# Optimization experiments

Hardware: AMD Instinct MI355X
Metric: run time of the kernel (lower is better)

## Reference

```python
import jax, jax.numpy as jnp
import numpy as np
import math

EMB, SEQ, OUT, FF, B = 1024, 1024, 2, 1024, 32
EPS = 1e-5


def _build_pe(seq_len, emb_dim):
    # Faithful to the buggy torch loop: for even i, pe[pos,i] is first set to sin
    # then immediately overwritten by cos(pos / 10000**(2*(i+1)/emb_dim));
    # odd indices are never written (stay 0).
    pos = np.arange(seq_len, dtype=np.float64)[:, None]
    i = np.arange(0, emb_dim, 2, dtype=np.float64)[None, :]
    pe = np.zeros((seq_len, emb_dim), dtype=np.float32)
    pe[:, ::2] = np.cos(pos / 10000.0 ** (2.0 * (i + 1.0) / emb_dim)).astype(np.float32)
    return jnp.asarray(pe)[None]  # [1, S, D]


def setup_inputs() -> dict:
    key = jax.random.key(0)
    ks = jax.random.split(key, 24)
    std = 0.02
    W = lambda k, o, i: jax.random.normal(k, (o, i), jnp.float32) * std
    b = lambda k, o: jax.random.normal(k, (o,), jnp.float32) * std
    return {
        "x": jax.random.normal(ks[0], (B, SEQ, EMB), jnp.float32),
        "pe": _build_pe(SEQ, EMB),
        "ln1_g": jnp.ones((EMB,), jnp.float32), "ln1_b": jnp.zeros((EMB,), jnp.float32),
        "Wq": W(ks[1], EMB, EMB), "bq": b(ks[2], EMB),
        "Wk": W(ks[3], EMB, EMB), "bk": b(ks[4], EMB),
        "Wv": W(ks[5], EMB, EMB), "bv": b(ks[6], EMB),
        "Wo": W(ks[7], EMB, EMB), "bo": b(ks[8], EMB),
        "ln2_g": jnp.ones((EMB,), jnp.float32), "ln2_b": jnp.zeros((EMB,), jnp.float32),
        "W1": W(ks[9], FF, EMB), "b1": b(ks[10], FF),
        "W2": W(ks[11], EMB, FF), "b2": b(ks[12], EMB),
        "Wc": W(ks[13], OUT, EMB), "bc": b(ks[14], OUT),
    }


def _ln(x, g, bias):
    mu = jnp.mean(x, axis=-1, keepdims=True)
    var = jnp.mean(jnp.square(x - mu), axis=-1, keepdims=True)
    return (x - mu) * jax.lax.rsqrt(var + EPS) * g + bias


def _block(x, ln1_g, ln1_b, Wq, bq, Wk, bk, Wv, bv, Wo, bo, ln2_g, ln2_b, W1, b1, W2, b2):
    h = _ln(x, ln1_g, ln1_b)
    q = h @ Wq.T + bq
    k = h @ Wk.T + bk
    v = h @ Wv.T + bv
    scores = jnp.einsum('bqd,bkd->bqk', q, k) / math.sqrt(EMB)
    w = jax.nn.softmax(scores, axis=-1)  # [B,S,S]
    attn = jnp.einsum('bqk,bkd->bqd', w, v) @ Wo.T + bo
    x2 = x + attn  # dropout is identity in eval
    h2 = _ln(x2, ln2_g, ln2_b)
    ff = jax.nn.relu(h2 @ W1.T + b1) @ W2.T + b2
    return x2 + ff, w


def reference(x, pe, ln1_g, ln1_b, Wq, bq, Wk, bk, Wv, bv, Wo, bo, ln2_g, ln2_b, W1, b1, W2, b2, Wc, bc):
    x1 = math.sqrt(EMB) * x + pe
    # Original forward applies block net2_1 twice (net2_2 is unused) -> reuse params.
    p = (ln1_g, ln1_b, Wq, bq, Wk, bk, Wv, bv, Wo, bo, ln2_g, ln2_b, W1, b1, W2, b2)
    x2_1, w1 = _block(x1, *p)
    x2_2, w2 = _block(x2_1, *p)
    logits = x2_2[:, 0, :] @ Wc.T + bc
    return logits, w1, w2
```

## Files before the change

kernel.cpp:

```cpp
#include <hip/hip_runtime.h>
#include <cstdint>


#define AS1 __attribute__((address_space(1)))
#define AS3 __attribute__((address_space(3)))

typedef __attribute__((ext_vector_type(8))) short bf16x8;
typedef __attribute__((ext_vector_type(4))) float f32x4;
typedef __attribute__((ext_vector_type(4))) unsigned short us4;

__device__ __forceinline__ unsigned short f2bf(float f) {
  unsigned int u = __builtin_bit_cast(unsigned int, f);
  u += 0x7fffu + ((u >> 16) & 1u);
  return (unsigned short)(u >> 16);
}
__device__ __forceinline__ float bf2f(unsigned short h) {
  return __builtin_bit_cast(float, (unsigned int)h << 16);
}

__device__ __forceinline__ void gload_lds16(const void* g, void* l) {
  auto gp = reinterpret_cast<AS1 unsigned int*>(reinterpret_cast<uintptr_t>(g));
  auto lp = reinterpret_cast<AS3 unsigned int*>(reinterpret_cast<uintptr_t>(l));
  __builtin_amdgcn_global_load_lds(gp, lp, 16, 0, 0);
}

enum { M_BF16 = 0, M_RELU = 1, M_QKV = 2, M_SCBF = 3, M_RESID = 4 };


#define MFMA_QUAD(qi, qj)                                                          \
  do {                                                                             \
    _Pragma("unroll") for (int i2 = 0; i2 < 4; ++i2) {                             \
      _Pragma("unroll") for (int j2 = 0; j2 < 2; ++j2) {                           \
        f32x4& c = acc[(qi) * 4 + i2][(qj) * 2 + j2];                              \
        c = __builtin_amdgcn_mfma_f32_16x16x32_bf16(aF[(qi) * 4 + i2][0],          \
                                                    bF[(qj) * 2 + j2][0], c, 0, 0, 0); \
        c = __builtin_amdgcn_mfma_f32_16x16x32_bf16(aF[(qi) * 4 + i2][1],          \
                                                    bF[(qj) * 2 + j2][1], c, 0, 0, 0); \
      }                                                                            \
    }                                                                              \
  } while (0)

template<int MODE>
__global__ __launch_bounds__(512, 2) void gemm_bt(
    const unsigned short* __restrict__ A, long long sAb,
    const unsigned short* __restrict__ B, long long sBb,
    const float* __restrict__ bias,
    const float* __restrict__ resid,
    float* __restrict__ outF,
    unsigned short* __restrict__ outBF,
    long long sOb, int N, int K, float scale)
{
  __shared__ __align__(16) unsigned short lds[65536];
  const int t    = threadIdx.x;
  const int w    = t >> 6;
  const int lane = t & 63;
  const int quad = lane >> 4;
  const int l16  = lane & 15;
  const int l7   = l16 & 7;
  const int wm   = w >> 2;
  const int wn   = w & 3;
  const int bz   = blockIdx.z;
  const unsigned short* Ab = A + (long long)bz * sAb;
  const unsigned short* Bb = B + (long long)bz * sBb;
  const int m0 = blockIdx.y * 256;
  const int n0 = blockIdx.x * 256;

  const int sr8  = lane >> 3;
  const int gseg = ((lane & 7) ^ sr8) << 3;
  const unsigned short* aSrc = Ab + (long long)(m0 + w * 8 + sr8) * K + gseg;
  const unsigned short* bSrc = Bb + (long long)(n0 + w * 8 + sr8) * K + gseg;
  const int ldsW = w << 9;

  const int aOff = (wm * 128 + l16) * 64;
  const int bOff = 16384 + (wn * 64 + l16) * 64;
  const int seg0 = (quad ^ l7) << 3;
  const int seg1 = ((quad + 4) ^ l7) << 3;

  const int NG = K >> 6;

  const f32x4 zero = {0.f, 0.f, 0.f, 0.f};
  f32x4 acc[8][4];
#pragma unroll
  for (int i = 0; i < 8; ++i)
#pragma unroll
    for (int j = 0; j < 4; ++j) acc[i][j] = zero;

  bf16x8 aF[8][2];
  bf16x8 bF[4][2];

#define STAGE_A(kt, h) do {                                                        \
    const unsigned short* _s = aSrc + (long long)(h) * 128 * K + (kt) * 64;        \
    unsigned short* _d = &lds[(((kt) & 1) << 15) + ((h) << 13) + ldsW];            \
    gload_lds16(_s, _d);                                                           \
    gload_lds16(_s + 64 * (long long)K, _d + 4096);                                \
  } while (0)
#define STAGE_B(kt, h) do {                                                        \
    const unsigned short* _s = bSrc + (long long)(h) * 128 * K + (kt) * 64;        \
    unsigned short* _d = &lds[(((kt) & 1) << 15) + 16384 + ((h) << 13) + ldsW];    \
    gload_lds16(_s, _d);                                                           \
    gload_lds16(_s + 64 * (long long)K, _d + 4096);                                \
  } while (0)

  STAGE_A(0, 0); STAGE_A(0, 1); STAGE_B(0, 0); STAGE_B(0, 1);
  STAGE_A(1, 0); STAGE_A(1, 1);
  asm volatile("s_waitcnt vmcnt(4)" ::: "memory");
  __builtin_amdgcn_s_barrier();
  asm volatile("" ::: "memory");

#pragma unroll 1
  for (int g = 0; g < NG; ++g) {
    const unsigned short* As = &lds[(g & 1) << 15];

#pragma unroll
    for (int i2 = 0; i2 < 4; ++i2) {
      aF[i2][0] = *(const bf16x8*)&As[aOff + i2 * 1024 + seg0];
      aF[i2][1] = *(const bf16x8*)&As[aOff + i2 * 1024 + seg1];
    }
#pragma unroll
    for (int j2 = 0; j2 < 2; ++j2) {
      bF[j2][0] = *(const bf16x8*)&As[bOff + j2 * 1024 + seg0];
      bF[j2][1] = *(const bf16x8*)&As[bOff + j2 * 1024 + seg1];
    }
    if (g + 1 < NG) STAGE_B(g + 1, 0);
    __builtin_amdgcn_s_barrier();
    asm volatile("s_waitcnt lgkmcnt(0)" ::: "memory");
    __builtin_amdgcn_s_setprio(1);
    MFMA_QUAD(0, 0);
    __builtin_amdgcn_s_setprio(0);
    __builtin_amdgcn_s_barrier();
    asm volatile("" ::: "memory");

#pragma unroll
    for (int i2 = 0; i2 < 4; ++i2) {
      aF[4 + i2][0] = *(const bf16x8*)&As[aOff + (4 + i2) * 1024 + seg0];
      aF[4 + i2][1] = *(const bf16x8*)&As[aOff + (4 + i2) * 1024 + seg1];
    }
    if (g + 1 < NG) STAGE_B(g + 1, 1);
    __builtin_amdgcn_s_barrier();
    asm volatile("s_waitcnt lgkmcnt(0)" ::: "memory");
    __builtin_amdgcn_s_setprio(1);
    MFMA_QUAD(1, 0);
    __builtin_amdgcn_s_setprio(0);
    __builtin_amdgcn_s_barrier();
    asm volatile("" ::: "memory");

#pragma unroll
    for (int j2 = 0; j2 < 2; ++j2) {
      bF[2 + j2][0] = *(const bf16x8*)&As[bOff + (2 + j2) * 1024 + seg0];
      bF[2 + j2][1] = *(const bf16x8*)&As[bOff + (2 + j2) * 1024 + seg1];
    }
    if (g + 2 < NG) STAGE_A(g + 2, 0);
    __builtin_amdgcn_s_barrier();
    asm volatile("s_waitcnt lgkmcnt(0)" ::: "memory");
    __builtin_amdgcn_s_setprio(1);
    MFMA_QUAD(1, 1);
    __builtin_amdgcn_s_setprio(0);
    __builtin_amdgcn_s_barrier();
    asm volatile("" ::: "memory");

    if (g + 2 < NG) STAGE_A(g + 2, 1);
    if (g >= NG - 2) {
      asm volatile("s_waitcnt vmcnt(0)" ::: "memory");
    } else {
      asm volatile("s_waitcnt vmcnt(4)" ::: "memory");
    }
    __builtin_amdgcn_s_barrier();
    __builtin_amdgcn_s_setprio(1);
    MFMA_QUAD(0, 1);
    __builtin_amdgcn_s_setprio(0);
    __builtin_amdgcn_s_barrier();
    asm volatile("" ::: "memory");
  }

#undef STAGE_A
#undef STAGE_B

#pragma unroll
  for (int i = 0; i < 8; ++i) {
    const int mt = m0 + wm * 128 + i * 16 + quad * 4;
#pragma unroll
    for (int j = 0; j < 4; ++j) {
      const int nt = n0 + wn * 64 + j * 16 + l16;
      f32x4 d = acc[i][j];
      if (MODE == M_BF16 || MODE == M_RELU) {
        const float bv = bias ? bias[nt] : 0.0f;
#pragma unroll
        for (int r = 0; r < 4; ++r) {
          float v = d[r] + bv;
          if (MODE == M_RELU) v = fmaxf(v, 0.0f);
          outBF[(long long)bz * sOb + (long long)(mt + r) * N + nt] = f2bf(v);
        }
      } else if (MODE == M_SCBF) {
#pragma unroll
        for (int r = 0; r < 4; ++r)
          outBF[(long long)bz * sOb + (long long)(mt + r) * N + nt] = f2bf(d[r] * scale);
      } else if (MODE == M_RESID) {
        const float bv = bias[nt];
#pragma unroll
        for (int r = 0; r < 4; ++r) {
          const long long idx = (long long)(mt + r) * N + nt;
          outF[idx] = resid[idx] + d[r] + bv;
        }
      } else if (MODE == M_QKV) {
        const int seg = n0 >> 10;
        const int ntl = nt - (seg << 10);
        const float bv = bias[nt];
        if (seg < 2) {
          unsigned short* dst = outBF + (long long)seg * 33554432LL;
#pragma unroll
          for (int r = 0; r < 4; ++r)
            dst[(long long)(mt + r) * 1024 + ntl] = f2bf(d[r] + bv);
        } else {
          unsigned short* dst = outBF + 2LL * 33554432LL;
          us4 pk;
#pragma unroll
          for (int r = 0; r < 4; ++r) pk[r] = f2bf(d[r] + bv);
          const int b = mt >> 10;
          const int s = mt & 1023;
          *(us4*)&dst[(long long)b * 1048576 + (long long)ntl * 1024 + s] = pk;
        }
      }
    }
  }
}

template<int EMBED>
__global__ __launch_bounds__(256) void ln_kernel(
    const float* __restrict__ xin, const float* __restrict__ pe,
    float* __restrict__ x1out,
    const float* __restrict__ g, const float* __restrict__ bb,
    unsigned short* __restrict__ hout)
{
  __shared__ float red[8];
  const long long row = blockIdx.x;
  const int t = threadIdx.x, lane = t & 63, w = t >> 6;
  float4 v = *(const float4*)(xin + row * 1024 + t * 4);
  if (EMBED) {
    const int s = (int)(row & 1023);
    float4 p = *(const float4*)(pe + (long long)s * 1024 + t * 4);
    v.x = 32.0f * v.x + p.x;
    v.y = 32.0f * v.y + p.y;
    v.z = 32.0f * v.z + p.z;
    v.w = 32.0f * v.w + p.w;
    *(float4*)(x1out + row * 1024 + t * 4) = v;
  }
  float sum = v.x + v.y + v.z + v.w;
  float sq  = v.x * v.x + v.y * v.y + v.z * v.z + v.w * v.w;
#pragma unroll
  for (int off = 32; off > 0; off >>= 1) {
    sum += __shfl_down(sum, off, 64);
    sq  += __shfl_down(sq,  off, 64);
  }
  if (lane == 0) { red[w] = sum; red[4 + w] = sq; }
  __syncthreads();
  sum = red[0] + red[1] + red[2] + red[3];
  sq  = red[4] + red[5] + red[6] + red[7];
  const float mu  = sum * (1.0f / 1024.0f);
  const float var = sq * (1.0f / 1024.0f) - mu * mu;
  const float rs  = rsqrtf(var + 1e-5f);
  float4 gg = *(const float4*)(g + t * 4);
  float4 bv = *(const float4*)(bb + t * 4);
  us4 h;
  h[0] = f2bf((v.x - mu) * rs * gg.x + bv.x);
  h[1] = f2bf((v.y - mu) * rs * gg.y + bv.y);
  h[2] = f2bf((v.z - mu) * rs * gg.z + bv.z);
  h[3] = f2bf((v.w - mu) * rs * gg.w + bv.w);
  *(us4*)(hout + row * 1024 + t * 4) = h;
}

__global__ __launch_bounds__(256) void softmax_kernel(
    const unsigned short* __restrict__ sbf,
    float* __restrict__ wout, unsigned short* __restrict__ wbf)
{
  __shared__ float red[8];
  const long long row = blockIdx.x;
  const int t = threadIdx.x, lane = t & 63, w = t >> 6;
  us4 sv = *(const us4*)(sbf + row * 1024 + t * 4);
  float4 v;
  v.x = bf2f(sv[0]); v.y = bf2f(sv[1]); v.z = bf2f(sv[2]); v.w = bf2f(sv[3]);
  float mx = fmaxf(fmaxf(v.x, v.y), fmaxf(v.z, v.w));
#pragma unroll
  for (int off = 32; off > 0; off >>= 1) mx = fmaxf(mx, __shfl_down(mx, off, 64));
  if (lane == 0) red[w] = mx;
  __syncthreads();
  mx = fmaxf(fmaxf(red[0], red[1]), fmaxf(red[2], red[3]));
  __syncthreads();
  const float e0 = __expf(v.x - mx), e1 = __expf(v.y - mx);
  const float e2 = __expf(v.z - mx), e3 = __expf(v.w - mx);
  float s = e0 + e1 + e2 + e3;
#pragma unroll
  for (int off = 32; off > 0; off >>= 1) s += __shfl_down(s, off, 64);
  if (lane == 0) red[w] = s;
  __syncthreads();
  s = red[0] + red[1] + red[2] + red[3];
  const float inv = 1.0f / s;
  float4 o; o.x = e0 * inv; o.y = e1 * inv; o.z = e2 * inv; o.w = e3 * inv;
  *(float4*)(wout + row * 1024 + t * 4) = o;
  us4 ob;
  ob[0] = f2bf(o.x); ob[1] = f2bf(o.y); ob[2] = f2bf(o.z); ob[3] = f2bf(o.w);
  *(us4*)(wbf + row * 1024 + t * 4) = ob;
}

__global__ __launch_bounds__(256) void prep_kernel(
    const float* __restrict__ Wq, const float* __restrict__ Wk, const float* __restrict__ Wv,
    const float* __restrict__ Wo, const float* __restrict__ W1, const float* __restrict__ W2,
    const float* __restrict__ bq, const float* __restrict__ bk, const float* __restrict__ bv,
    unsigned short* __restrict__ qkvw, unsigned short* __restrict__ Wo_bf,
    unsigned short* __restrict__ W1_bf, unsigned short* __restrict__ W2_bf,
    float* __restrict__ qkvb)
{
  const int y = blockIdx.y;
  const long long i = blockIdx.x * 256 + threadIdx.x;
  if (y == 6) {
    if (i < 768) {
      const float* src = (i < 256) ? bq : (i < 512) ? bk : bv;
      float4 v = *(const float4*)(src + (i & 255) * 4);
      *(float4*)(qkvb + i * 4) = v;
    }
    return;
  }
  const float* src;
  unsigned short* dst;
  switch (y) {
    case 0: src = Wq; dst = qkvw;            break;
    case 1: src = Wk; dst = qkvw + 1048576;  break;
    case 2: src = Wv; dst = qkvw + 2097152;  break;
    case 3: src = Wo; dst = Wo_bf;           break;
    case 4: src = W1; dst = W1_bf;           break;
    default: src = W2; dst = W2_bf;          break;
  }
  float4 v = *(const float4*)(src + i * 4);
  us4 o;
  o[0] = f2bf(v.x); o[1] = f2bf(v.y); o[2] = f2bf(v.z); o[3] = f2bf(v.w);
  *(us4*)(dst + i * 4) = o;
}

__global__ __launch_bounds__(256) void logits_kernel(
    const float* __restrict__ x, const float* __restrict__ Wc,
    const float* __restrict__ bc, float* __restrict__ out)
{
  __shared__ float red[4];
  const int blk = blockIdx.x;
  const int b = blk >> 1, o = blk & 1;
  const int t = threadIdx.x, lane = t & 63, w = t >> 6;
  const float* xr = x + (long long)b * 1048576;
  const float* wr = Wc + o * 1024;
  float4 xv = *(const float4*)(xr + t * 4);
  float4 wv = *(const float4*)(wr + t * 4);
  float s = xv.x * wv.x + xv.y * wv.y + xv.z * wv.z + xv.w * wv.w;
#pragma unroll
  for (int off = 32; off > 0; off >>= 1) s += __shfl_down(s, off, 64);
  if (lane == 0) red[w] = s;
  __syncthreads();
  if (t == 0) out[blk] = red[0] + red[1] + red[2] + red[3] + bc[o];
}

extern "C" void kernel_launch(void* const* d_in, const int* in_sizes, int n_in,
                              void* d_out, int out_size, void* d_ws, size_t ws_size,
                              hipStream_t stream)
{
  const float* x    = (const float*)d_in[0];
  const float* pe   = (const float*)d_in[1];
  const float* ln1g = (const float*)d_in[2];
  const float* ln1b = (const float*)d_in[3];
  const float* Wq   = (const float*)d_in[4];
  const float* bq   = (const float*)d_in[5];
  const float* Wk   = (const float*)d_in[6];
  const float* bk   = (const float*)d_in[7];
  const float* Wv   = (const float*)d_in[8];
  const float* bv   = (const float*)d_in[9];
  const float* Wo   = (const float*)d_in[10];
  const float* bo   = (const float*)d_in[11];
  const float* ln2g = (const float*)d_in[12];
  const float* ln2b = (const float*)d_in[13];
  const float* W1   = (const float*)d_in[14];
  const float* b1   = (const float*)d_in[15];
  const float* W2   = (const float*)d_in[16];
  const float* b2   = (const float*)d_in[17];
  const float* Wc   = (const float*)d_in[18];
  const float* bc   = (const float*)d_in[19];
  float* out = (float*)d_out;

  char* ws = (char*)d_ws;
  float*          xbuf  = (float*)ws;
  unsigned short* h_bf  = (unsigned short*)(ws + 134217728LL);
  unsigned short* q_bf  = (unsigned short*)(ws + 134217728LL + 1 * 67108864LL);
  unsigned short* k_bf  = (unsigned short*)(ws + 134217728LL + 2 * 67108864LL);
  unsigned short* vT_bf = (unsigned short*)(ws + 134217728LL + 3 * 67108864LL);
  unsigned short* wts   = (unsigned short*)(ws + 134217728LL + 4 * 67108864LL);
  unsigned short* QKV_bf = wts;
  unsigned short* Wo_bf  = wts + 3LL * 1048576;
  unsigned short* W1_bf  = wts + 4LL * 1048576;
  unsigned short* W2_bf  = wts + 5LL * 1048576;
  float*          qkvb   = (float*)(wts + 6LL * 1048576);
  unsigned short* sc_bf   = h_bf;
  unsigned short* w_bf    = k_bf;
  unsigned short* attn_bf = q_bf;
  unsigned short* ff1_bf  = vT_bf;

  const dim3 blk(256);
  const dim3 blkG(512);
  prep_kernel<<<dim3(1024, 7), blk, 0, stream>>>(Wq, Wk, Wv, Wo, W1, W2, bq, bk, bv,
                                                 QKV_bf, Wo_bf, W1_bf, W2_bf, qkvb);

  const dim3 gQKV(12, 128, 1);
  const dim3 gProj(4, 128, 1);
  const dim3 gAttn(4, 4, 32);

  for (int blkI = 0; blkI < 2; ++blkI) {
    float* wslot = out + 64 + (long long)blkI * 33554432LL;

    if (blkI == 0)
      ln_kernel<1><<<32768, blk, 0, stream>>>(x, pe, xbuf, ln1g, ln1b, h_bf);
    else
      ln_kernel<0><<<32768, blk, 0, stream>>>(xbuf, nullptr, nullptr, ln1g, ln1b, h_bf);

    gemm_bt<M_QKV><<<gQKV, blkG, 0, stream>>>(h_bf, 0, QKV_bf, 0, qkvb, nullptr,
                                              nullptr, q_bf, 0, 3072, 1024, 1.0f);

    gemm_bt<M_SCBF><<<gAttn, blkG, 0, stream>>>(q_bf, 1048576, k_bf, 1048576, nullptr,
                                                nullptr, nullptr, sc_bf, 1048576,
                                                1024, 1024, 0.03125f);
    softmax_kernel<<<32768, blk, 0, stream>>>(sc_bf, wslot, w_bf);

    gemm_bt<M_BF16><<<gAttn, blkG, 0, stream>>>(w_bf, 1048576, vT_bf, 1048576, nullptr,
                                                nullptr, nullptr, attn_bf, 1048576,
                                                1024, 1024, 1.0f);
    gemm_bt<M_RESID><<<gProj, blkG, 0, stream>>>(attn_bf, 0, Wo_bf, 0, bo, xbuf,
                                                 xbuf, nullptr, 0, 1024, 1024, 1.0f);

    ln_kernel<0><<<32768, blk, 0, stream>>>(xbuf, nullptr, nullptr, ln2g, ln2b, h_bf);
    gemm_bt<M_RELU><<<gProj, blkG, 0, stream>>>(h_bf, 0, W1_bf, 0, b1, nullptr,
                                                nullptr, ff1_bf, 0, 1024, 1024, 1.0f);
    gemm_bt<M_RESID><<<gProj, blkG, 0, stream>>>(ff1_bf, 0, W2_bf, 0, b2, xbuf,
                                                 xbuf, nullptr, 0, 1024, 1024, 1.0f);
  }

  logits_kernel<<<64, blk, 0, stream>>>(xbuf, Wc, bc, out);
  (void)in_sizes; (void)n_in; (void)out_size; (void)ws_size;
}
```

Before: 1.936 ms.

## Software-pipeline LDS fragment reads across MFMA quads and stage bf16 epilogue through LDS

Restructures the GEMM main loop so LDS fragment reads for the next quad, and for the next k-tile, are issued before the current MFMA quad runs. This halves the barriers per quad and unrolls the loop by two with explicit buffer offsets. The bf16 output epilogue now writes the tile into swizzled LDS and then emits 16-byte coalesced global stores instead of scattered 2-byte stores. The risks are LDS hazards from reusing the operand buffer for the epilogue and tighter vmcnt accounting, and the two-way unroll assumes an even NG.

New measurement: 3.079 ms. 1.59x slower.

```diff
diff --git a/kernel.cpp b/kernel.cpp
--- a/kernel.cpp
+++ b/kernel.cpp
@@ -8,6 +8,7 @@
 typedef __attribute__((ext_vector_type(8))) short bf16x8;
 typedef __attribute__((ext_vector_type(4))) float f32x4;
 typedef __attribute__((ext_vector_type(4))) unsigned short us4;
+typedef __attribute__((ext_vector_type(8))) unsigned short us8;
 
 __device__ __forceinline__ unsigned short f2bf(float f) {
   unsigned int u = __builtin_bit_cast(unsigned int, f);
@@ -25,7 +26,6 @@
 }
 
 enum { M_BF16 = 0, M_RELU = 1, M_QKV = 2, M_SCBF = 3, M_RESID = 4 };
-
 
 #define MFMA_QUAD(qi, qj)                                                          \
   do {                                                                             \
@@ -88,137 +88,172 @@
   bf16x8 aF[8][2];
   bf16x8 bF[4][2];
 
-#define STAGE_A(kt, h) do {                                                        \
+#define STAGE_A(kt, h, SL) do {                                                    \
     const unsigned short* _s = aSrc + (long long)(h) * 128 * K + (kt) * 64;        \
-    unsigned short* _d = &lds[(((kt) & 1) << 15) + ((h) << 13) + ldsW];            \
+    unsigned short* _d = &lds[(SL) + ((h) << 13) + ldsW];                          \
     gload_lds16(_s, _d);                                                           \
     gload_lds16(_s + 64 * (long long)K, _d + 4096);                                \
   } while (0)
-#define STAGE_B(kt, h) do {                                                        \
+#define STAGE_B(kt, h, SL) do {                                                    \
     const unsigned short* _s = bSrc + (long long)(h) * 128 * K + (kt) * 64;        \
-    unsigned short* _d = &lds[(((kt) & 1) << 15) + 16384 + ((h) << 13) + ldsW];    \
+    unsigned short* _d = &lds[(SL) + 16384 + ((h) << 13) + ldsW];                  \
     gload_lds16(_s, _d);                                                           \
     gload_lds16(_s + 64 * (long long)K, _d + 4096);                                \
   } while (0)
 
-  STAGE_A(0, 0); STAGE_A(0, 1); STAGE_B(0, 0); STAGE_B(0, 1);
-  STAGE_A(1, 0); STAGE_A(1, 1);
+#define READ_A03(SL)                                                               \
+    _Pragma("unroll") for (int i2 = 0; i2 < 4; ++i2) {                             \
+      aF[i2][0] = *(const bf16x8*)&lds[(SL) + aOff + i2 * 1024 + seg0];            \
+      aF[i2][1] = *(const bf16x8*)&lds[(SL) + aOff + i2 * 1024 + seg1];            \
+    }
+#define READ_A47(SL)                                                               \
+    _Pragma("unroll") for (int i2 = 0; i2 < 4; ++i2) {                             \
+      aF[4 + i2][0] = *(const bf16x8*)&lds[(SL) + aOff + (4 + i2) * 1024 + seg0];  \
+      aF[4 + i2][1] = *(const bf16x8*)&lds[(SL) + aOff + (4 + i2) * 1024 + seg1];  \
+    }
+#define READ_B01(SL)                                                               \
+    _Pragma("unroll") for (int j2 = 0; j2 < 2; ++j2) {                             \
+      bF[j2][0] = *(const bf16x8*)&lds[(SL) + bOff + j2 * 1024 + seg0];            \
+      bF[j2][1] = *(const bf16x8*)&lds[(SL) + bOff + j2 * 1024 + seg1];            \
+    }
+#define READ_B23(SL)                                                               \
+    _Pragma("unroll") for (int j2 = 0; j2 < 2; ++j2) {                             \
+      bF[2 + j2][0] = *(const bf16x8*)&lds[(SL) + bOff + (2 + j2) * 1024 + seg0];  \
+      bF[2 + j2][1] = *(const bf16x8*)&lds[(SL) + bOff + (2 + j2) * 1024 + seg1];  \
+    }
+
+#define KTILE(g, CUR, OTH)                                                         \
+  {                            \
+    __builtin_amdgcn_s_barrier();                                                  \
+    if ((g) + 1 < NG) STAGE_B((g) + 1, 0, OTH);                                    \
+    READ_B23(CUR)                                                                  \
+    __builtin_amdgcn_s_setprio(1);                                                 \
+    MFMA_QUAD(0, 0);                                                               \
+    __builtin_amdgcn_s_setprio(0);                                                 \
+    asm volatile("s_waitcnt lgkmcnt(0)" ::: "memory");                             \
+  }                                                                                \
+  {                                              \
+    __builtin_amdgcn_s_barrier();                                                  \
+    if ((g) + 1 < NG) STAGE_B((g) + 1, 1, OTH);                                    \
+    READ_A47(CUR)                                                                  \
+    __builtin_amdgcn_s_setprio(1);                                                 \
+    MFMA_QUAD(0, 1);                                                               \
+    __builtin_amdgcn_s_setprio(0);                                                 \
+    asm volatile("s_waitcnt lgkmcnt(0)" ::: "memory");                             \
+  }                                                                                \
+  {                                              \
+    __builtin_amdgcn_s_barrier();                                                  \
+    if ((g) + 2 < NG) STAGE_A((g) + 2, 0, CUR);                                    \
+    __builtin_amdgcn_s_setprio(1);                                                 \
+    MFMA_QUAD(1, 0);                                                               \
+    __builtin_amdgcn_s_setprio(0);                                                 \
+    if ((g) + 2 < NG) {                                                            \
+      asm volatile("s_waitcnt vmcnt(2) lgkmcnt(0)" ::: "memory");                  \
+    } else {                                                                       \
+      asm volatile("s_waitcnt vmcnt(0) lgkmcnt(0)" ::: "memory");                  \
+    }                                                                              \
+  }                                                                                \
+  {     \
+    __builtin_amdgcn_s_barrier();                                                  \
+    if ((g) + 2 < NG) STAGE_A((g) + 2, 1, CUR);                                    \
+    if ((g) + 1 < NG) {                                                            \
+      READ_A03(OTH)                                                                \
+      READ_B01(OTH)                                                                \
+    }                                                                              \
+    __builtin_amdgcn_s_setprio(1);                                                 \
+    MFMA_QUAD(1, 1);                                                               \
+    __builtin_amdgcn_s_setprio(0);                                                 \
+    asm volatile("s_waitcnt lgkmcnt(0)" ::: "memory");                             \
+  }
+
+  STAGE_A(0, 0, 0); STAGE_A(0, 1, 0); STAGE_B(0, 0, 0); STAGE_B(0, 1, 0);
+  STAGE_A(1, 0, 32768); STAGE_A(1, 1, 32768);
   asm volatile("s_waitcnt vmcnt(4)" ::: "memory");
   __builtin_amdgcn_s_barrier();
-  asm volatile("" ::: "memory");
+  READ_A03(0)
+  READ_B01(0)
+  asm volatile("s_waitcnt lgkmcnt(0)" ::: "memory");
 
 #pragma unroll 1
-  for (int g = 0; g < NG; ++g) {
-    const unsigned short* As = &lds[(g & 1) << 15];
-
-#pragma unroll
-    for (int i2 = 0; i2 < 4; ++i2) {
-      aF[i2][0] = *(const bf16x8*)&As[aOff + i2 * 1024 + seg0];
-      aF[i2][1] = *(const bf16x8*)&As[aOff + i2 * 1024 + seg1];
-    }
-#pragma unroll
-    for (int j2 = 0; j2 < 2; ++j2) {
-      bF[j2][0] = *(const bf16x8*)&As[bOff + j2 * 1024 + seg0];
-      bF[j2][1] = *(const bf16x8*)&As[bOff + j2 * 1024 + seg1];
-    }
-    if (g + 1 < NG) STAGE_B(g + 1, 0);
-    __builtin_amdgcn_s_barrier();
-    asm volatile("s_waitcnt lgkmcnt(0)" ::: "memory");
-    __builtin_amdgcn_s_setprio(1);
-    MFMA_QUAD(0, 0);
-    __builtin_amdgcn_s_setprio(0);
-    __builtin_amdgcn_s_barrier();
-    asm volatile("" ::: "memory");
-
-#pragma unroll
-    for (int i2 = 0; i2 < 4; ++i2) {
-      aF[4 + i2][0] = *(const bf16x8*)&As[aOff + (4 + i2) * 1024 + seg0];
-      aF[4 + i2][1] = *(const bf16x8*)&As[aOff + (4 + i2) * 1024 + seg1];
-    }
-    if (g + 1 < NG) STAGE_B(g + 1, 1);
-    __builtin_amdgcn_s_barrier();
-    asm volatile("s_waitcnt lgkmcnt(0)" ::: "memory");
-    __builtin_amdgcn_s_setprio(1);
-    MFMA_QUAD(1, 0);
-    __builtin_amdgcn_s_setprio(0);
-    __builtin_amdgcn_s_barrier();
-    asm volatile("" ::: "memory");
-
-#pragma unroll
-    for (int j2 = 0; j2 < 2; ++j2) {
-      bF[2 + j2][0] = *(const bf16x8*)&As[bOff + (2 + j2) * 1024 + seg0];
-      bF[2 + j2][1] = *(const bf16x8*)&As[bOff + (2 + j2) * 1024 + seg1];
-    }
-    if (g + 2 < NG) STAGE_A(g + 2, 0);
-    __builtin_amdgcn_s_barrier();
-    asm volatile("s_waitcnt lgkmcnt(0)" ::: "memory");
-    __builtin_amdgcn_s_setprio(1);
-    MFMA_QUAD(1, 1);
-    __builtin_amdgcn_s_setprio(0);
-    __builtin_amdgcn_s_barrier();
-    asm volatile("" ::: "memory");
-
-    if (g + 2 < NG) STAGE_A(g + 2, 1);
-    if (g >= NG - 2) {
-      asm volatile("s_waitcnt vmcnt(0)" ::: "memory");
-    } else {
-      asm volatile("s_waitcnt vmcnt(4)" ::: "memory");
-    }
-    __builtin_amdgcn_s_barrier();
-    __builtin_amdgcn_s_setprio(1);
-    MFMA_QUAD(0, 1);
-    __builtin_amdgcn_s_setprio(0);
-    __builtin_amdgcn_s_barrier();
-    asm volatile("" ::: "memory");
-  }
-
+  for (int g = 0; g < NG; g += 2) {
+    KTILE(g, 0, 32768)
+    KTILE(g + 1, 32768, 0)
+  }
+
+#undef KTILE
 #undef STAGE_A
 #undef STAGE_B
 
-#pragma unroll
-  for (int i = 0; i < 8; ++i) {
-    const int mt = m0 + wm * 128 + i * 16 + quad * 4;
-#pragma unroll
-    for (int j = 0; j < 4; ++j) {
-      const int nt = n0 + wn * 64 + j * 16 + l16;
-      f32x4 d = acc[i][j];
-      if (MODE == M_BF16 || MODE == M_RELU) {
-        const float bv = bias ? bias[nt] : 0.0f;
-#pragma unroll
-        for (int r = 0; r < 4; ++r) {
-          float v = d[r] + bv;
-          if (MODE == M_RELU) v = fmaxf(v, 0.0f);
-          outBF[(long long)bz * sOb + (long long)(mt + r) * N + nt] = f2bf(v);
-        }
-      } else if (MODE == M_SCBF) {
-#pragma unroll
-        for (int r = 0; r < 4; ++r)
-          outBF[(long long)bz * sOb + (long long)(mt + r) * N + nt] = f2bf(d[r] * scale);
-      } else if (MODE == M_RESID) {
+  const int segq = (MODE == M_QKV) ? (n0 >> 10) : 0;
+  if (MODE == M_QKV && segq == 2) {
+#pragma unroll
+    for (int i = 0; i < 8; ++i) {
+      const int mt = m0 + wm * 128 + i * 16 + quad * 4;
+#pragma unroll
+      for (int j = 0; j < 4; ++j) {
+        const int nt = n0 + wn * 64 + j * 16 + l16;
+        const int ntl = nt - 2048;
         const float bv = bias[nt];
+        f32x4 d = acc[i][j];
+        unsigned short* dst = outBF + 2LL * 33554432LL;
+        us4 pk;
+#pragma unroll
+        for (int r = 0; r < 4; ++r) pk[r] = f2bf(d[r] + bv);
+        const int b = mt >> 10;
+        const int s = mt & 1023;
+        *(us4*)&dst[(long long)b * 1048576 + (long long)ntl * 1024 + s] = pk;
+      }
+    }
+  } else if (MODE == M_RESID) {
+#pragma unroll
+    for (int i = 0; i < 8; ++i) {
+      const int mt = m0 + wm * 128 + i * 16 + quad * 4;
+#pragma unroll
+      for (int j = 0; j < 4; ++j) {
+        const int nt = n0 + wn * 64 + j * 16 + l16;
+        const float bv = bias[nt];
+        f32x4 d = acc[i][j];
 #pragma unroll
         for (int r = 0; r < 4; ++r) {
           const long long idx = (long long)(mt + r) * N + nt;
           outF[idx] = resid[idx] + d[r] + bv;
         }
-      } else if (MODE == M_QKV) {
-        const int seg = n0 >> 10;
-        const int ntl = nt - (seg << 10);
-        const float bv = bias[nt];
-        if (seg < 2) {
-          unsigned short* dst = outBF + (long long)seg * 33554432LL;
-#pragma unroll
-          for (int r = 0; r < 4; ++r)
-            dst[(long long)(mt + r) * 1024 + ntl] = f2bf(d[r] + bv);
-        } else {
-          unsigned short* dst = outBF + 2LL * 33554432LL;
-          us4 pk;
-#pragma unroll
-          for (int r = 0; r < 4; ++r) pk[r] = f2bf(d[r] + bv);
-          const int b = mt >> 10;
-          const int s = mt & 1023;
-          *(us4*)&dst[(long long)b * 1048576 + (long long)ntl * 1024 + s] = pk;
+      }
+    }
+  } else {
+#pragma unroll
+    for (int i = 0; i < 8; ++i) {
+      const int lr0 = wm * 128 + i * 16 + quad * 4;
+#pragma unroll
+      for (int j = 0; j < 4; ++j) {
+        const int colg = wn * 64 + j * 16 + l16;
+        float bv = 0.0f;
+        if (MODE == M_BF16 || MODE == M_RELU || MODE == M_QKV)
+          bv = bias ? bias[n0 + colg] : 0.0f;
+        f32x4 d = acc[i][j];
+#pragma unroll
+        for (int r = 0; r < 4; ++r) {
+          float v;
+          if (MODE == M_SCBF) v = d[r] * scale;
+          else                v = d[r] + bv;
+          if (MODE == M_RELU) v = fmaxf(v, 0.0f);
+          const int lr = lr0 + r;
+          lds[lr * 256 + (colg ^ ((lr & 7) << 3))] = f2bf(v);
         }
+      }
+    }
+    __syncthreads();
+    const int lr = t >> 1;
+    const int cb = (t & 1) * 128;
+#pragma unroll
+    for (int k = 0; k < 16; ++k) {
+      const int colg = cb + k * 8;
+      us8 vv = *(const us8*)&lds[lr * 256 + (colg ^ ((lr & 7) << 3))];
+      if (MODE == M_QKV) {
+        unsigned short* dst = outBF + (long long)segq * 33554432LL;
+        *(us8*)&dst[(long long)(m0 + lr) * 1024 + (n0 + colg - (segq << 10))] = vv;
+      } else {
+        *(us8*)&outBF[(long long)bz * sOb + (long long)(m0 + lr) * N + (n0 + colg)] = vv;
       }
     }
   }
```
